# Optimization experiments

Hardware: AMD Instinct MI355X
Metric: run time of the kernel (lower is better)

The kernel has to match this reference:

```python
import jax, jax.numpy as jnp
import numpy as np

D_MANIFOLD = 1024
D_FIBER = 512


def setup_inputs() -> dict:
    key = jax.random.key(0)
    ks = jax.random.split(key, 9)
    B, SQ, SK = 4, 4096, 4096
    m_states = jax.random.normal(ks[0], (B, SQ, D_MANIFOLD), dtype=jnp.float32)
    f_states_k = jax.random.normal(ks[1], (B, SK, D_FIBER), dtype=jnp.float32)
    f_states_v = jax.random.normal(ks[2], (B, SK, D_FIBER), dtype=jnp.float32)
    s_q = 1.0 / np.sqrt(D_MANIFOLD)
    s_f = 1.0 / np.sqrt(D_FIBER)
    W_q = jax.random.uniform(ks[3], (D_MANIFOLD, D_FIBER), jnp.float32, -s_q, s_q)
    b_q = jax.random.uniform(ks[4], (D_FIBER,), jnp.float32, -s_q, s_q)
    W_k = jax.random.uniform(ks[5], (D_FIBER, D_FIBER), jnp.float32, -s_f, s_f)
    b_k = jax.random.uniform(ks[6], (D_FIBER,), jnp.float32, -s_f, s_f)
    W_v = jax.random.uniform(ks[7], (D_FIBER, D_FIBER), jnp.float32, -s_f, s_f)
    b_v = jax.random.uniform(ks[8], (D_FIBER,), jnp.float32, -s_f, s_f)
    return {
        "m_states": m_states,
        "f_states_k": f_states_k,
        "f_states_v": f_states_v,
        "W_q": W_q, "b_q": b_q,
        "W_k": W_k, "b_k": b_k,
        "W_v": W_v, "b_v": b_v,
    }


def reference(m_states, f_states_k, f_states_v, W_q, b_q, W_k, b_k, W_v, b_v):
    scale = D_FIBER ** (-0.5)
    Q = jnp.einsum("bsm,md->bsd", m_states, W_q) + b_q   # [B,SQ,Df]
    K = jnp.einsum("btf,fd->btd", f_states_k, W_k) + b_k  # [B,SK,Df]
    V = jnp.einsum("btf,fd->btd", f_states_v, W_v) + b_v  # [B,SK,Df]
    scores = jnp.einsum("bsd,btd->bst", Q, K) * scale     # [B,SQ,SK]
    weights = jax.nn.softmax(scores, axis=-1)
    return jnp.einsum("bst,btd->bsd", weights, V)         # [B,SQ,Df]
```

## Files before the change

### kernel.cpp

```cpp
#include <hip/hip_runtime.h>


typedef __attribute__((ext_vector_type(8)))  short short8;
typedef __attribute__((ext_vector_type(16))) float f32x16;
typedef __attribute__((ext_vector_type(4)))  float float4v;

__device__ __forceinline__ short f2bf(float x){
  unsigned int u = __float_as_uint(x);
  u = (u + 0x7FFFu + ((u >> 16) & 1u)) >> 16;
  return (short)u;
}

__device__ __forceinline__ unsigned cvt_pk_bf16(float a, float b){
  unsigned r;
  asm("v_cvt_pk_bf16_f32 %0, %1, %2" : "=v"(r) : "v"(a), "v"(b));
  return r;
}

__device__ __forceinline__ float fast_exp2(float x){
  float r; asm("v_exp_f32 %0, %1" : "=v"(r) : "v"(x)); return r;
}

__device__ __forceinline__ void bar_lgkm(){
  asm volatile("s_waitcnt lgkmcnt(0)" ::: "memory");
  __builtin_amdgcn_s_barrier();
}

typedef const __attribute__((address_space(1))) unsigned int guint_t;
typedef __attribute__((address_space(3))) unsigned int luint_t;
__device__ __forceinline__ void gl_lds16(const void* g, void* l){
  __builtin_amdgcn_global_load_lds((guint_t*)g, (luint_t*)l, 16, 0, 0);
}

__global__ __launch_bounds__(256) void transpose_cvt_fused(
    const float* __restrict__ Wq, const float* __restrict__ Wk,
    const float* __restrict__ Wv,
    short* __restrict__ WqT, short* __restrict__ WkT, short* __restrict__ WvT)
{
  int idx = blockIdx.x * 256 + threadIdx.x;
  if (idx < 524288){
    int n = idx & 511, k = idx >> 9;
    WqT[(n<<10) + k] = f2bf(Wq[idx]);
  } else if (idx < 786432){
    int j = idx - 524288; int n = j & 511, k = j >> 9;
    WkT[(n<<9) + k] = f2bf(Wk[j]);
  } else {
    int j = idx - 786432; int n = j & 511, k = j >> 9;
    WvT[(n<<9) + k] = f2bf(Wv[j]);
  }
}

__global__ __launch_bounds__(256, 2) void proj_gemm_fused(
    const float* __restrict__ Aq, const float* __restrict__ Ak,
    const float* __restrict__ Av,
    const short* __restrict__ Wq, const short* __restrict__ Wk,
    const short* __restrict__ Wv,
    const float* __restrict__ bq, const float* __restrict__ bk,
    const float* __restrict__ bv,
    short* __restrict__ Cq, short* __restrict__ Ck, short* __restrict__ Cv,
    float scale)
{
  __shared__ char As[16384];
  __shared__ char Bs[16384];
  const int pz = blockIdx.z;
  const float* A    = (pz==0) ? Aq : (pz==1) ? Ak : Av;
  const short* WT   = (pz==0) ? Wq : (pz==1) ? Wk : Wv;
  const float* bias = (pz==0) ? bq : (pz==1) ? bk : bv;
  short* C          = (pz==0) ? Cq : (pz==1) ? Ck : Cv;
  const int K       = (pz==0) ? 1024 : 512;
  const float alpha = (pz==0) ? scale : 1.0f;

  const int tid = threadIdx.x;
  const int wid = tid >> 6, lane = tid & 63;
  const int lo = lane & 31, hi = lane >> 5;
  const int wm = wid >> 1, wn = wid & 1;
  const int bm = blockIdx.x, bn = blockIdx.y;
  const char* WTb = (const char*)WT;

  f32x16 acc[2][2];
  #pragma unroll
  for (int i=0;i<2;i++)
    #pragma unroll
    for (int j=0;j<2;j++)
      #pragma unroll
      for (int r=0;r<16;r++) acc[i][j][r] = 0.0f;

  const int srow = tid >> 3, sslot = tid & 7;
  const int aswz = (sslot*16) ^ ((srow&7)<<4);
  for (int k0 = 0; k0 < K; k0 += 64) {
    #pragma unroll
    for (int i=0;i<4;i++){
      const int rb0 = wid*32 + i*8;
      const int rr = lane >> 3;
      const void* src = WTb + ((size_t)(bn*128 + rb0 + rr)*K + k0)*2
                        + (((lane&7)*16) ^ (rr<<4));
      gl_lds16(src, Bs + rb0*128);
    }
    #pragma unroll
    for (int i=0;i<4;i++){
      const int row = srow + 32*i;
      const float4v* src = (const float4v*)&A[(size_t)(bm*128+row)*K + k0 + sslot*8];
      float4v f0 = src[0], f1 = src[1];
      uint4 u;
      u.x = cvt_pk_bf16(f0[0], f0[1]);
      u.y = cvt_pk_bf16(f0[2], f0[3]);
      u.z = cvt_pk_bf16(f1[0], f1[1]);
      u.w = cvt_pk_bf16(f1[2], f1[3]);
      *(uint4*)(As + row*128 + aswz) = u;
    }
    __syncthreads();
    #pragma unroll
    for (int dc=0; dc<4; dc++){
      short8 af[2], bfr[2];
      #pragma unroll
      for (int mt=0;mt<2;mt++){
        const int ra = wm*64+mt*32+lo;
        af[mt] = *(const short8*)(As + ra*128 + ((dc*32 + hi*16) ^ ((ra&7)<<4)));
      }
      #pragma unroll
      for (int nt=0;nt<2;nt++){
        const int rb = wn*64+nt*32+lo;
        bfr[nt] = *(const short8*)(Bs + rb*128 + ((dc*32 + hi*16) ^ ((rb&7)<<4)));
      }
      #pragma unroll
      for (int mt=0;mt<2;mt++)
        #pragma unroll
        for (int nt=0;nt<2;nt++)
          acc[mt][nt] = __builtin_amdgcn_mfma_f32_32x32x16_bf16(af[mt], bfr[nt], acc[mt][nt], 0, 0, 0);
    }
    __syncthreads();
  }

  char* Cb = (char*)C;
  #pragma unroll
  for (int nt=0;nt<2;nt++){
    const int col = bn*128 + wn*64 + nt*32 + lo;
    const float bv2 = bias[col];
    #pragma unroll
    for (int mt=0;mt<2;mt++){
      const int grow0 = bm*128 + wm*64 + mt*32;
      if (pz == 0){
        #pragma unroll
        for (int r=0;r<16;r++){
          const int t = grow0 + (r&3) + 8*(r>>2) + 4*hi;
          const int d = col;
          const float val = (acc[mt][nt][r] + bv2) * alpha;
          size_t addr = (size_t)(t>>6)*65536
                      + (size_t)((d>>5)*4 + ((d>>4)&1)*2 + ((d>>3)&1))*1024
                      + (size_t)(t&63)*16 + (d&7)*2;
          *(short*)(Cb + addr) = f2bf(val);
        }
      } else if (pz == 1){
        #pragma unroll
        for (int r=0;r<16;r++){
          const int t = grow0 + (r&3) + 8*(r>>2) + 4*hi;
          const int d = col;
          const float val = acc[mt][nt][r] + bv2;
          size_t addr = (size_t)(t>>9)*524288 + (size_t)((t>>5)&15)*32768
                      + (size_t)((d>>5)*2 + ((d>>4)&1))*1024
                      + (size_t)((t&31) + 32*((d>>3)&1))*16 + (d&7)*2;
          *(short*)(Cb + addr) = f2bf(val);
        }
      } else {
        #pragma unroll
        for (int r=0;r<16;r++){
          const int t = grow0 + (r&3) + 8*(r>>2) + 4*hi;
          const int d = col;
          const float val = acc[mt][nt][r] + bv2;
          size_t addr = (size_t)(t>>9)*524288 + (size_t)(d>>6)*65536
                      + (size_t)(((d>>5)&1)*32 + ((t>>4)&31))*1024
                      + (size_t)((d&31) + 32*((t>>3)&1))*16 + (t&7)*2;
          *(short*)(Cb + addr) = f2bf(val);
        }
      }
    }
  }
}

#define PLDS  65536
#define LSUMO 131072
#define ALDS  133120

__global__ __launch_bounds__(512, 2) void attn_fwd(
    const char* __restrict__ Qg, const char* __restrict__ Kf,
    const char* __restrict__ Vf, float* __restrict__ out)
{
  extern __shared__ char smem[];
  float* lsum_lds = (float*)(smem + LSUMO);

  const int tid = threadIdx.x;
  const int w = tid >> 6, lane = tid & 63;
  const int lo = lane & 31, hi = lane >> 5;
  const int wg = ((blockIdx.x & 7) << 5) + (blockIdx.x >> 3);
  const int b = wg >> 6, qt = wg & 63;
  const size_t qrow0 = ((size_t)b << 12) + (size_t)qt*64;

  const int qbase  = hi*1024 + lo*16;
  const int prbase = PLDS + hi*1024 + lo*16;
  const int pwbase = PLDS + (w<<13) + lo*16 + hi*8;

  {
    const char* qsrc = Qg + (size_t)wg*65536;
    #pragma unroll
    for (int i=0;i<8;i++)
      gl_lds16(qsrc + (w*8+i)*1024 + lane*16, smem + (w*8+i)*1024);
  }

  f32x16 oacc[2][2];
  #pragma unroll
  for (int i=0;i<2;i++)
    #pragma unroll
    for (int j=0;j<2;j++)
      #pragma unroll
      for (int r=0;r<16;r++) oacc[i][j][r]=0.f;
  float ls[2] = {0.f, 0.f};

  const char* Kb = Kf + (size_t)b*4194304;
  const char* Vb = Vf + (size_t)b*4194304;
  short8 kfb[2][8], vfb[2][8];

  {
    const char* kbase0 = Kb + (size_t)(2*w)*32768 + (size_t)lane*16;
    #pragma unroll
    for (int kvsub=0;kvsub<2;kvsub++)
      #pragma unroll
      for (int dc2=0;dc2<2;dc2++)
        #pragma unroll
        for (int ks=0;ks<2;ks++)
          kfb[0][kvsub*4+dc2*2+ks] = *(const short8*)(kbase0
              + (size_t)kvsub*32768 + dc2*2048 + ks*1024);
  }
  __syncthreads();

  for (int kvt = 0; kvt < 8; kvt++) {
    const bool last = (kvt == 7);
    const char* kbaseC = Kb + (size_t)kvt*524288 + (size_t)(2*w)*32768 + (size_t)lane*16;
    const char* kbaseN = Kb + (size_t)((kvt+1)&7)*524288 + (size_t)(2*w)*32768 + (size_t)lane*16;
    const char* vbase  = Vb + (size_t)kvt*524288 + (size_t)(w)*65536 + (size_t)lane*16;

    f32x16 sacc[2][2];
    #pragma unroll
    for (int i=0;i<2;i++)
      #pragma unroll
      for (int j=0;j<2;j++)
        #pragma unroll
        for (int r=0;r<16;r++) sacc[i][j][r]=0.f;

    #pragma unroll
    for (int g=0; g<8; g++){
      const int bf = g & 1;
      if (g < 7){
        #pragma unroll
        for (int kvsub=0;kvsub<2;kvsub++)
          #pragma unroll
          for (int dc2=0;dc2<2;dc2++)
            #pragma unroll
            for (int ks=0;ks<2;ks++)
              kfb[bf^1][kvsub*4+dc2*2+ks] = *(const short8*)(kbaseC
                  + (size_t)kvsub*32768 + (2*(g+1)+dc2)*2048 + ks*1024);
      }
      __builtin_amdgcn_s_setprio(1);
      #pragma unroll
      for (int dc2=0;dc2<2;dc2++)
        #pragma unroll
        for (int ks=0;ks<2;ks++){
          const int dch = 2*g + dc2;
          short8 qf[2];
          #pragma unroll
          for (int qs=0;qs<2;qs++)
            qf[qs] = *(const short8*)(smem + qbase + dch*4096 + ks*2048 + qs*512);
          #pragma unroll
          for (int kvsub=0;kvsub<2;kvsub++)
            #pragma unroll
            for (int qs=0;qs<2;qs++)
              sacc[kvsub][qs] = __builtin_amdgcn_mfma_f32_32x32x16_bf16(
                  kfb[bf][kvsub*4+dc2*2+ks], qf[qs], sacc[kvsub][qs], 0, 0, 0);
        }
      __builtin_amdgcn_s_setprio(0);
    }

    #pragma unroll
    for (int dsub=0;dsub<2;dsub++)
      #pragma unroll
      for (int ts=0;ts<4;ts++)
        vfb[0][dsub*4+ts] = *(const short8*)(vbase + (size_t)dsub*32768 + ts*1024);

    #pragma unroll
    for (int kvsub=0;kvsub<2;kvsub++)
      #pragma unroll
      for (int qs=0;qs<2;qs++){
        #pragma unroll
        for (int g4=0; g4<4; g4++){
          float p0 = fast_exp2(sacc[kvsub][qs][4*g4+0]);
          float p1 = fast_exp2(sacc[kvsub][qs][4*g4+1]);
          float p2 = fast_exp2(sacc[kvsub][qs][4*g4+2]);
          float p3 = fast_exp2(sacc[kvsub][qs][4*g4+3]);
          ls[qs] += (p0 + p1) + (p2 + p3);
          uint2 pv;
          pv.x = cvt_pk_bf16(p0, p1);
          pv.y = cvt_pk_bf16(p2, p3);
          *(uint2*)(smem + pwbase + kvsub*4096 + g4*1024 + qs*512) = pv;
        }
      }
    bar_lgkm();

    #pragma unroll
    for (int g=0; g<8; g++){
      const int bf = g & 1;
      if (g < 7){
        #pragma unroll
        for (int dsub=0;dsub<2;dsub++)
          #pragma unroll
          for (int ts=0;ts<4;ts++)
            vfb[bf^1][dsub*4+ts] = *(const short8*)(vbase
                + (size_t)dsub*32768 + ((g+1)*4+ts)*1024);
      }
      __builtin_amdgcn_s_setprio(1);
      #pragma unroll
      for (int ts=0; ts<4; ts++){
        const int tst = g*4 + ts;
        short8 pf[2];
        #pragma unroll
        for (int qs=0;qs<2;qs++)
          pf[qs] = *(const short8*)(smem + prbase + tst*2048 + qs*512);
        #pragma unroll
        for (int dsub=0;dsub<2;dsub++)
          #pragma unroll
          for (int qs=0;qs<2;qs++)
            oacc[dsub][qs] = __builtin_amdgcn_mfma_f32_32x32x16_bf16(
                vfb[bf][dsub*4+ts], pf[qs], oacc[dsub][qs], 0, 0, 0);
      }
      __builtin_amdgcn_s_setprio(0);
    }

    if (!last){
      #pragma unroll
      for (int kvsub=0;kvsub<2;kvsub++)
        #pragma unroll
        for (int dc2=0;dc2<2;dc2++)
          #pragma unroll
          for (int ks=0;ks<2;ks++)
            kfb[0][kvsub*4+dc2*2+ks] = *(const short8*)(kbaseN
                + (size_t)kvsub*32768 + dc2*2048 + ks*1024);
    }
    bar_lgkm();
  }

  ls[0] += __shfl_xor(ls[0], 32);
  ls[1] += __shfl_xor(ls[1], 32);
  if (hi == 0){
    lsum_lds[w*64 + lo]      = ls[0];
    lsum_lds[w*64 + 32 + lo] = ls[1];
  }
  __syncthreads();

  #pragma unroll
  for (int qs=0;qs<2;qs++){
    float l_tot = 0.f;
    #pragma unroll
    for (int wv=0;wv<8;wv++) l_tot += lsum_lds[wv*64 + qs*32 + lo];
    const float inv = 1.0f / l_tot;
    const size_t row = qrow0 + qs*32 + lo;
    #pragma unroll
    for (int dsub=0;dsub<2;dsub++){
      #pragma unroll
      for (int g4=0;g4<4;g4++){
        float4v ov;
        #pragma unroll
        for (int j=0;j<4;j++) ov[j] = oacc[dsub][qs][4*g4+j]*inv;
        *(float4v*)&out[row*512 + w*64 + dsub*32 + g4*8 + hi*4] = ov;
      }
    }
  }
}

extern "C" void kernel_launch(void* const* d_in, const int* in_sizes, int n_in,
                              void* d_out, int out_size, void* d_ws, size_t ws_size,
                              hipStream_t stream)
{
  const float* m_states = (const float*)d_in[0];
  const float* f_k      = (const float*)d_in[1];
  const float* f_v      = (const float*)d_in[2];
  const float* W_q      = (const float*)d_in[3];
  const float* b_q      = (const float*)d_in[4];
  const float* W_k      = (const float*)d_in[5];
  const float* b_k      = (const float*)d_in[6];
  const float* W_v      = (const float*)d_in[7];
  const float* b_v      = (const float*)d_in[8];
  float* out = (float*)d_out;

  char* ws = (char*)d_ws;
  short* WqT = (short*)(ws);
  short* WkT = (short*)(ws + 1048576);
  short* WvT = (short*)(ws + 1048576 + 524288);
  short* Qb  = (short*)(ws + 2097152);
  short* Kfr = Qb + (size_t)16384*512;
  short* Vfr = Kfr + (size_t)16384*512;

  transpose_cvt_fused<<<4096, 256, 0, stream>>>(W_q, W_k, W_v, WqT, WkT, WvT);

  const float scale = 0.044194173824159216f * 1.4426950408889634f;
  proj_gemm_fused<<<dim3(128,4,3), 256, 0, stream>>>(
      m_states, f_k, f_v, WqT, WkT, WvT, b_q, b_k, b_v,
      Qb, Kfr, Vfr, scale);

  attn_fwd<<<256, 512, ALDS, stream>>>((const char*)Qb, (const char*)Kfr,
                                       (const char*)Vfr, out);
}
```

Before: 195.3 us.

## Retile projection GEMM to 64x512 block tiles so each A row loads once

The projection GEMM now uses a 64-row by full-512-column tile per block, with each wave owning 128 output columns. The grid drops to 256x3 blocks. The fp32 activation tile is read and converted to bf16 exactly once rather than four times, one per column block. In exchange, LDS use rises to 72KB per block, which lowers occupancy, and each block stages a much larger weight tile every k step.

```diff
diff --git a/kernel.cpp b/kernel.cpp
--- a/kernel.cpp
+++ b/kernel.cpp
@@ -60,9 +60,9 @@
     short* __restrict__ Cq, short* __restrict__ Ck, short* __restrict__ Cv,
     float scale)
 {
-  __shared__ char As[16384];
-  __shared__ char Bs[16384];
-  const int pz = blockIdx.z;
+  __shared__ char As[8192];
+  __shared__ char Bs[65536];
+  const int pz = blockIdx.y;
   const float* A    = (pz==0) ? Aq : (pz==1) ? Ak : Av;
   const short* WT   = (pz==0) ? Wq : (pz==1) ? Wk : Wv;
   const float* bias = (pz==0) ? bq : (pz==1) ? bk : bv;
@@ -73,59 +73,61 @@
   const int tid = threadIdx.x;
   const int wid = tid >> 6, lane = tid & 63;
   const int lo = lane & 31, hi = lane >> 5;
-  const int wm = wid >> 1, wn = wid & 1;
-  const int bm = blockIdx.x, bn = blockIdx.y;
+  const int bm = blockIdx.x;
   const char* WTb = (const char*)WT;
 
-  f32x16 acc[2][2];
+  f32x16 acc[2][4];
   #pragma unroll
   for (int i=0;i<2;i++)
     #pragma unroll
-    for (int j=0;j<2;j++)
+    for (int j=0;j<4;j++)
       #pragma unroll
       for (int r=0;r<16;r++) acc[i][j][r] = 0.0f;
 
-  const int srow = tid >> 3, sslot = tid & 7;
-  const int aswz = (sslot*16) ^ ((srow&7)<<4);
+  const int srow = tid >> 2, sslot = tid & 3;
   for (int k0 = 0; k0 < K; k0 += 64) {
     #pragma unroll
-    for (int i=0;i<4;i++){
-      const int rb0 = wid*32 + i*8;
+    for (int i=0;i<16;i++){
+      const int rb0 = wid*128 + i*8;
       const int rr = lane >> 3;
-      const void* src = WTb + ((size_t)(bn*128 + rb0 + rr)*K + k0)*2
+      const void* src = WTb + ((size_t)(rb0 + rr)*K + k0)*2
                         + (((lane&7)*16) ^ (rr<<4));
       gl_lds16(src, Bs + rb0*128);
     }
-    #pragma unroll
-    for (int i=0;i<4;i++){
-      const int row = srow + 32*i;
-      const float4v* src = (const float4v*)&A[(size_t)(bm*128+row)*K + k0 + sslot*8];
-      float4v f0 = src[0], f1 = src[1];
-      uint4 u;
-      u.x = cvt_pk_bf16(f0[0], f0[1]);
-      u.y = cvt_pk_bf16(f0[2], f0[3]);
-      u.z = cvt_pk_bf16(f1[0], f1[1]);
-      u.w = cvt_pk_bf16(f1[2], f1[3]);
-      *(uint4*)(As + row*128 + aswz) = u;
+    {
+      const float4v* src = (const float4v*)&A[(size_t)(bm*64+srow)*K + k0 + sslot*16];
+      float4v f0 = src[0], f1 = src[1], f2 = src[2], f3 = src[3];
+      uint4 u0, u1;
+      u0.x = cvt_pk_bf16(f0[0], f0[1]);
+      u0.y = cvt_pk_bf16(f0[2], f0[3]);
+      u0.z = cvt_pk_bf16(f1[0], f1[1]);
+      u0.w = cvt_pk_bf16(f1[2], f1[3]);
+      u1.x = cvt_pk_bf16(f2[0], f2[1]);
+      u1.y = cvt_pk_bf16(f2[2], f2[3]);
+      u1.z = cvt_pk_bf16(f3[0], f3[1]);
+      u1.w = cvt_pk_bf16(f3[2], f3[3]);
+      const int swz = (srow&7)<<4;
+      *(uint4*)(As + srow*128 + ((sslot*32)      ^ swz)) = u0;
+      *(uint4*)(As + srow*128 + ((sslot*32 + 16) ^ swz)) = u1;
     }
     __syncthreads();
     #pragma unroll
     for (int dc=0; dc<4; dc++){
-      short8 af[2], bfr[2];
+      short8 af[2], bfr[4];
       #pragma unroll
       for (int mt=0;mt<2;mt++){
-        const int ra = wm*64+mt*32+lo;
+        const int ra = mt*32+lo;
         af[mt] = *(const short8*)(As + ra*128 + ((dc*32 + hi*16) ^ ((ra&7)<<4)));
       }
       #pragma unroll
-      for (int nt=0;nt<2;nt++){
-        const int rb = wn*64+nt*32+lo;
+      for (int nt=0;nt<4;nt++){
+        const int rb = wid*128 + nt*32 + lo;
         bfr[nt] = *(const short8*)(Bs + rb*128 + ((dc*32 + hi*16) ^ ((rb&7)<<4)));
       }
       #pragma unroll
       for (int mt=0;mt<2;mt++)
         #pragma unroll
-        for (int nt=0;nt<2;nt++)
+        for (int nt=0;nt<4;nt++)
           acc[mt][nt] = __builtin_amdgcn_mfma_f32_32x32x16_bf16(af[mt], bfr[nt], acc[mt][nt], 0, 0, 0);
     }
     __syncthreads();
@@ -133,12 +135,12 @@
 
   char* Cb = (char*)C;
   #pragma unroll
-  for (int nt=0;nt<2;nt++){
-    const int col = bn*128 + wn*64 + nt*32 + lo;
+  for (int nt=0;nt<4;nt++){
+    const int col = wid*128 + nt*32 + lo;
     const float bv2 = bias[col];
     #pragma unroll
     for (int mt=0;mt<2;mt++){
-      const int grow0 = bm*128 + wm*64 + mt*32;
+      const int grow0 = bm*64 + mt*32;
       if (pz == 0){
         #pragma unroll
         for (int r=0;r<16;r++){
@@ -400,7 +402,7 @@
   transpose_cvt_fused<<<4096, 256, 0, stream>>>(W_q, W_k, W_v, WqT, WkT, WvT);
 
   const float scale = 0.044194173824159216f * 1.4426950408889634f;
-  proj_gemm_fused<<<dim3(128,4,3), 256, 0, stream>>>(
+  proj_gemm_fused<<<dim3(256,3), 256, 0, stream>>>(
       m_states, f_k, f_v, WqT, WkT, WvT, b_q, b_k, b_v,
       Qb, Kfr, Vfr, scale);
 
```

After: 196.1 us. About the same (+0.4%).
